# Performance work log

Hardware: AMD Instinct MI355X
Metric: run time of the kernel (lower is better)

The kernel has to match this reference:

```python
import jax, jax.numpy as jnp
import numpy as np

N = 4096  # nmentions
# Static index sets: strict lower triangle in row-major order (matches torch
# boolean-mask assignment order) and the diagonal.
ROWS, COLS = np.tril_indices(N, -1)
DIAG = np.arange(N)


def setup_inputs() -> dict:
    key = jax.random.key(0)
    k1, k2, k3 = jax.random.split(key, 3)
    eps_scores = jax.random.normal(k1, (N,), dtype=jnp.float32)
    ana_scores = jax.random.normal(k2, (N * (N - 1) // 2,), dtype=jnp.float32)
    # Build a coherent solution mask: random cluster ids; a mention's correct
    # antecedents are earlier mentions of the same cluster, else itself (epsilon).
    clusters = np.asarray(jax.random.randint(k3, (N,), 0, N // 8))
    same = clusters[:, None] == clusters[None, :]
    lower = np.tril(np.ones((N, N), dtype=bool), -1)
    sol_link = same & lower
    has_ante = sol_link.any(axis=1)
    mask = sol_link.astype(np.float32)
    mask[DIAG, DIAG] = (~has_ante).astype(np.float32)
    link_costs = jnp.array([[0.5], [1.0]], dtype=jnp.float32)  # [false_link],[wrong_link]
    false_new_cost = jnp.array([1.5], dtype=jnp.float32)
    return {
        "eps_scores": eps_scores,
        "ana_scores": ana_scores,
        "solution_mask": jnp.asarray(mask),
        "link_costs": link_costs,
        "false_new_cost": false_new_cost,
    }


def create_score_matrix(eps_scores, ana_scores):
    # [N,N]: diagonal = epsilon (non-anaphoric) scores, strict lower triangle =
    # pairwise antecedent scores in row-major tril order; upper triangle zero.
    scores = jnp.zeros((N, N), dtype=eps_scores.dtype)
    scores = scores.at[DIAG, DIAG].set(eps_scores)
    scores = scores.at[ROWS, COLS].set(ana_scores)
    return scores


def reference(eps_scores, ana_scores, solution_mask, link_costs, false_new_cost):
    scores = create_score_matrix(eps_scores, ana_scores)
    minimum_score = scores.min()
    solution_scores = solution_mask * scores + (1.0 - solution_mask) * minimum_score
    best_correct = solution_scores.max(axis=1)  # [N]
    non_anaphoric = jnp.diagonal(solution_mask)  # [N]
    # anaphoricity_selector @ link_costs.expand(2, N): each row is a constant
    # equal to false_link if non-anaphoric else wrong_link.
    row_cost = non_anaphoric * link_costs[0, 0] + (1.0 - non_anaphoric) * link_costs[1, 0]
    potential_costs = jnp.tril(jnp.broadcast_to(row_cost[:, None], (N, N)), -1)
    potential_costs = potential_costs.at[DIAG, DIAG].set(false_new_cost[0])
    cost_matrix = (1.0 - solution_mask) * potential_costs
    loss_values = cost_matrix * (1.0 + scores - best_correct[:, None])
    loss_per_example = loss_values.max(axis=1)  # [N]
    return loss_per_example
```

## Files before the change

### kernel.cpp

```cpp
#include <hip/hip_runtime.h>

#define N 4096
#define BLK 256

__global__ __launch_bounds__(BLK) void mention_loss_kernel(
    const float* __restrict__ eps_scores,
    const float* __restrict__ ana_scores,
    const float* __restrict__ mask,
    const float* __restrict__ link_costs,
    const float* __restrict__ false_new_cost,
    float* __restrict__ out)
{
    const int row = N - 1 - (int)blockIdx.x;
    __shared__ float s_score[N];
    __shared__ float s_mask[N];
    __shared__ float s_red[BLK / 64];
    __shared__ float s_bc;

    const int tid = threadIdx.x;
    const long long base = (long long)row * (row - 1) / 2;
    const float* mrow = mask + (size_t)row * N;

    float bc = -INFINITY;
    for (int j = tid; j <= row; j += BLK) {
        float s = (j < row) ? ana_scores[base + j] : eps_scores[row];
        float m = mrow[j];
        s_score[j] = s;
        s_mask[j]  = m;
        if (m != 0.0f) bc = fmaxf(bc, s);
    }
    for (int off = 32; off; off >>= 1) bc = fmaxf(bc, __shfl_down(bc, off));
    if ((tid & 63) == 0) s_red[tid >> 6] = bc;
    __syncthreads();
    if (tid == 0) {
        float v = s_red[0];
        for (int w = 1; w < BLK / 64; ++w) v = fmaxf(v, s_red[w]);
        s_bc = v;
    }
    __syncthreads();

    const float bcv = s_bc;
    const float lc0 = link_costs[0];
    const float lc1 = link_costs[1];
    const float fn  = false_new_cost[0];
    const float d   = s_mask[row];
    const float rc  = d * lc0 + (1.0f - d) * lc1;

    float loss = 0.0f;
    for (int j = tid; j <= row; j += BLK) {
        float pc = (j == row) ? fn : rc;
        float c  = (1.0f - s_mask[j]) * pc;
        loss = fmaxf(loss, c * (1.0f + s_score[j] - bcv));
    }
    for (int off = 32; off; off >>= 1) loss = fmaxf(loss, __shfl_down(loss, off));
    if ((tid & 63) == 0) s_red[tid >> 6] = loss;
    __syncthreads();
    if (tid == 0) {
        float v = s_red[0];
        for (int w = 1; w < BLK / 64; ++w) v = fmaxf(v, s_red[w]);
        out[row] = v;
    }
}

extern "C" void kernel_launch(void* const* d_in, const int* in_sizes, int n_in,
                              void* d_out, int out_size, void* d_ws, size_t ws_size,
                              hipStream_t stream) {
    const float* eps  = (const float*)d_in[0];
    const float* ana  = (const float*)d_in[1];
    const float* mask = (const float*)d_in[2];
    const float* lc   = (const float*)d_in[3];
    const float* fnc  = (const float*)d_in[4];
    float* out = (float*)d_out;

    mention_loss_kernel<<<N, BLK, 0, stream>>>(eps, ana, mask, lc, fnc, out);
}
```

Baseline: 131.5 us.

## Collapse two-pass row loss into single pass tracking max unmasked score

The two-pass scheme (stage the row in shared memory, then recompute the loss per element) is replaced by one streaming pass. It keeps two running maxima: the best masked score and the best unmasked score. Since the row cost is constant over off-diagonal entries, the loss can be rebuilt from these two maxima plus the diagonal term. The loop is fully unrolled over N/BLK iterations with a bound guard, which drops the shared-memory staging and one barrier, at the cost of a differently handled empty-row edge case.

```diff
diff --git a/kernel.cpp b/kernel.cpp
--- a/kernel.cpp
+++ b/kernel.cpp
@@ -12,53 +12,44 @@
     float* __restrict__ out)
 {
     const int row = N - 1 - (int)blockIdx.x;
-    __shared__ float s_score[N];
-    __shared__ float s_mask[N];
-    __shared__ float s_red[BLK / 64];
-    __shared__ float s_bc;
-
     const int tid = threadIdx.x;
     const long long base = (long long)row * (row - 1) / 2;
-    const float* mrow = mask + (size_t)row * N;
+    const float* __restrict__ mrow = mask + (size_t)row * (size_t)N;
 
-    float bc = -INFINITY;
-    for (int j = tid; j <= row; j += BLK) {
-        float s = (j < row) ? ana_scores[base + j] : eps_scores[row];
-        float m = mrow[j];
-        s_score[j] = s;
-        s_mask[j]  = m;
-        if (m != 0.0f) bc = fmaxf(bc, s);
+    float bc  = -3.4e38f;
+    float sm0 = -3.4e38f;
+
+#pragma unroll
+    for (int it = 0; it < N / BLK; ++it) {
+        const int j = tid + it * BLK;
+        if (j < row) {
+            const float s = ana_scores[base + j];
+            const float m = mrow[j];
+            if (m != 0.0f) bc  = fmaxf(bc,  s);
+            else           sm0 = fmaxf(sm0, s);
+        }
     }
-    for (int off = 32; off; off >>= 1) bc = fmaxf(bc, __shfl_down(bc, off));
-    if ((tid & 63) == 0) s_red[tid >> 6] = bc;
+
+    for (int off = 32; off; off >>= 1) {
+        bc  = fmaxf(bc,  __shfl_down(bc,  off));
+        sm0 = fmaxf(sm0, __shfl_down(sm0, off));
+    }
+    __shared__ float r_bc[BLK / 64], r_sm[BLK / 64];
+    if ((tid & 63) == 0) { r_bc[tid >> 6] = bc; r_sm[tid >> 6] = sm0; }
     __syncthreads();
     if (tid == 0) {
-        float v = s_red[0];
-        for (int w = 1; w < BLK / 64; ++w) v = fmaxf(v, s_red[w]);
-        s_bc = v;
-    }
-    __syncthreads();
-
-    const float bcv = s_bc;
-    const float lc0 = link_costs[0];
-    const float lc1 = link_costs[1];
-    const float fn  = false_new_cost[0];
-    const float d   = s_mask[row];
-    const float rc  = d * lc0 + (1.0f - d) * lc1;
-
-    float loss = 0.0f;
-    for (int j = tid; j <= row; j += BLK) {
-        float pc = (j == row) ? fn : rc;
-        float c  = (1.0f - s_mask[j]) * pc;
-        loss = fmaxf(loss, c * (1.0f + s_score[j] - bcv));
-    }
-    for (int off = 32; off; off >>= 1) loss = fmaxf(loss, __shfl_down(loss, off));
-    if ((tid & 63) == 0) s_red[tid >> 6] = loss;
-    __syncthreads();
-    if (tid == 0) {
-        float v = s_red[0];
-        for (int w = 1; w < BLK / 64; ++w) v = fmaxf(v, s_red[w]);
-        out[row] = v;
+        float B = r_bc[0], S = r_sm[0];
+        for (int w = 1; w < BLK / 64; ++w) {
+            B = fmaxf(B, r_bc[w]);
+            S = fmaxf(S, r_sm[w]);
+        }
+        const float e = eps_scores[row];
+        const float d = mrow[row];
+        if (d != 0.0f) B = fmaxf(B, e);
+        const float rc = d * link_costs[0] + (1.0f - d) * link_costs[1];
+        float loss = fmaxf(0.0f, rc * (1.0f + S - B));
+        if (d == 0.0f) loss = fmaxf(loss, false_new_cost[0] * (1.0f + e - B));
+        out[row] = loss;
     }
 }
 
```

Result: faster. 121.1 us (-7.9%).
